# Performance work log

Hardware: AMD Instinct MI355X
Metric: run time of the kernel (lower is better)

## Reference

```python
import jax, jax.numpy as jnp
from jax import lax
import numpy as np

B, T, IN, H = 4096, 200, 79, 10  # batch, seq_len, input_size, hidden_size


def setup_inputs() -> dict:
    key = jax.random.key(0)
    ks = jax.random.split(key, 12)
    f32 = jnp.float32
    return {
        "x": jax.random.normal(ks[0], (B, T, IN), f32),
        # BayesianLSTM reparameterized params: W = mu + softplus(rho) * eps
        "wih_mu": jax.random.normal(ks[1], (IN, 4 * H), f32) * 0.1,
        "wih_rho": jnp.full((IN, 4 * H), -3.0, f32),
        "wih_eps": jax.random.normal(ks[2], (IN, 4 * H), f32),
        "whh_mu": jax.random.normal(ks[3], (H, 4 * H), f32) * 0.1,
        "whh_rho": jnp.full((H, 4 * H), -3.0, f32),
        "whh_eps": jax.random.normal(ks[4], (H, 4 * H), f32),
        "b_mu": jax.random.normal(ks[5], (4 * H,), f32) * 0.1,
        "b_rho": jnp.full((4 * H,), -3.0, f32),
        "b_eps": jax.random.normal(ks[6], (4 * H,), f32),
        # deterministic linear head (10 -> 1)
        "lin_w": jax.random.normal(ks[7], (H, 1), f32) * 0.3,
        "lin_b": jax.random.normal(ks[8], (1,), f32) * 0.1,
    }


def reference(x, wih_mu, wih_rho, wih_eps, whh_mu, whh_rho, whh_eps,
              b_mu, b_rho, b_eps, lin_w, lin_b):
    sp = jax.nn.softplus
    Wih = wih_mu + sp(wih_rho) * wih_eps   # [IN, 4H]
    Whh = whh_mu + sp(whh_rho) * whh_eps   # [H, 4H]
    b = b_mu + sp(b_rho) * b_eps           # [4H]

    # Precompute input projection for all timesteps: [T, B, 4H]
    xg = jnp.einsum('bti,ig->tbg', x, Wih) + b

    h0 = jnp.zeros((x.shape[0], Whh.shape[0]), x.dtype)
    c0 = h0

    def step(carry, g_t):
        h, c = carry
        gates = g_t + h @ Whh
        i, f, g, o = jnp.split(gates, 4, axis=-1)
        i = jax.nn.sigmoid(i)
        f = jax.nn.sigmoid(f)
        g = jnp.tanh(g)
        o = jax.nn.sigmoid(o)
        c = f * c + i * g
        h = o * jnp.tanh(c)
        return (h, c), None

    (hT, _), _ = lax.scan(step, (h0, c0), xg)
    # x_[:, -1, :] == final hidden state hT; then linear head
    return hT @ lin_w + lin_b  # [B, 1]
```

## Files before the change

kernel.cpp:

```cpp
#include <hip/hip_runtime.h>
#include <cstdint>
#include <cmath>

#define Bsz 4096
#define Tlen 200
#define INs 79
#define Hs 10
#define Gs 40
#define LOG2E 1.4426950408889634f

typedef __attribute__((ext_vector_type(8))) short bf16x8;
typedef __attribute__((ext_vector_type(4))) float f32x4;

__device__ __forceinline__ unsigned short f2bf(float x) {
    unsigned u = __float_as_uint(x);
    return (unsigned short)((u + 0x7FFF + ((u >> 16) & 1)) >> 16);
}

__global__ void prep_kernel(const float* __restrict__ wih_mu, const float* __restrict__ wih_rho, const float* __restrict__ wih_eps,
                            const float* __restrict__ whh_mu, const float* __restrict__ whh_rho, const float* __restrict__ whh_eps,
                            const float* __restrict__ b_mu,   const float* __restrict__ b_rho,   const float* __restrict__ b_eps,
                            float* __restrict__ w) {
    int idx = blockIdx.x * 256 + threadIdx.x;
    if (idx < 4608) {
        int c = idx / 96, k = idx % 96;
        float val = 0.0f;
        if (c < Gs && k < INs) {
            int s = k * Gs + c;
            float r = wih_rho[s];
            float sp = (r > 20.0f) ? r : log1pf(expf(r));
            val = fmaf(sp, wih_eps[s], wih_mu[s]);
            val *= (c >= 20 && c < 30) ? -2.0f : -1.0f;
        }
        unsigned short h = f2bf(val);
        float back = __uint_as_float((unsigned)h << 16);
        unsigned short l = f2bf(val - back);
        ((unsigned short*)(w + 512))[idx]  = h;
        ((unsigned short*)(w + 2816))[idx] = l;
    } else if (idx < 5008) {
        int m = idx - 4608;
        float r = whh_rho[m];
        float sp = (r > 20.0f) ? r : log1pf(expf(r));
        w[48 + m] = fmaf(sp, whh_eps[m], whh_mu[m]);
    } else if (idx < 5056) {
        int m = idx - 5008;
        float val = 0.0f;
        if (m < Gs) {
            float r = b_rho[m];
            float sp = (r > 20.0f) ? r : log1pf(expf(r));
            val = fmaf(sp, b_eps[m], b_mu[m]);
            val *= (m >= 20 && m < 30) ? -2.0f : -1.0f;
        }
        w[m] = val;
    }
}

__global__ __launch_bounds__(64, 4) void fused_kernel(
    const float* __restrict__ x, const float* __restrict__ w,
    const float* __restrict__ lin_w, const float* __restrict__ lin_b,
    float* __restrict__ out) {
    __shared__ __align__(16) float sm[1280 + 16 * 42];
    float* xbuf = sm;
    float* gbuf = sm + 1280;

    const int b = blockIdx.x;
    const int lane = threadIdx.x;
    const int jj = lane & 15;
    const int kg8 = (lane >> 4) * 8;

    if (lane < 16) sm[1264 + lane] = 0.0f;

    const unsigned short* Bh = (const unsigned short*)(w + 512);
    const unsigned short* Bl = (const unsigned short*)(w + 2816);

    int pj = (lane & 3) * 10 + (lane >> 2); if (pj > 39) pj = 39;
    const int ty = lane & 3;
    const float sAL = ((ty == 2) ? -2.0f : -1.0f) * LOG2E;
    const float sM  = (ty == 2) ? (-4.0f * LOG2E) : 1.0f;
    const float sC  = (ty == 2) ? ( 2.0f * LOG2E) : 0.0f;
    float wcs[Hs];
#pragma unroll
    for (int k = 0; k < Hs; ++k) wcs[k] = w[48 + k * Gs + pj] * sAL;
    float bias3[3];
#pragma unroll
    for (int n = 0; n < 3; ++n) bias3[n] = w[n * 16 + jj];

    float hs[Hs];
#pragma unroll
    for (int k = 0; k < Hs; ++k) hs[k] = 0.0f;
    float C = 0.0f;

    const long xbaseB = (long)b * (Tlen * INs) * 4;
    const long xendB  = (long)Bsz * Tlen * INs * 4 - 16;
    auto* ldsc = (__attribute__((address_space(3))) char*)xbuf;

    auto stage = [&](int t0) {
        long srcB = xbaseB + (long)t0 * INs * 4;
#pragma unroll
        for (int kk = 0; kk < 4; ++kk) {
            long off = srcB + (long)(kk * 64 + lane) * 16;
            if (off > xendB) off = xendB;
            __builtin_amdgcn_global_load_lds(
                (const __attribute__((address_space(1))) void*)((const char*)x + off),
                (__attribute__((address_space(3))) void*)(ldsc + (kk * 64 + lane) * 16), 16, 0, 0);
        }
        if (lane < 60) {
            long off = srcB + (long)(256 + lane) * 16;
            if (off > xendB) off = xendB;
            __builtin_amdgcn_global_load_lds(
                (const __attribute__((address_space(1))) void*)((const char*)x + off),
                (__attribute__((address_space(3))) void*)(ldsc + (256 + lane) * 16), 16, 0, 0);
        }
    };

    stage(0);

    for (int tile = 0; tile < 13; ++tile) {
        const int t0 = tile * 16;
        asm volatile("s_waitcnt vmcnt(0)" ::: "memory");

        float f0[8], f1[8], f2[8];
#pragma unroll
        for (int e = 0; e < 8; ++e) f0[e] = xbuf[jj * INs + kg8 + e];
#pragma unroll
        for (int e = 0; e < 8; ++e) f1[e] = xbuf[jj * INs + 32 + kg8 + e];
#pragma unroll
        for (int e = 0; e < 8; ++e) {
            float raw = xbuf[jj * INs + 64 + kg8 + e];
            f2[e] = (kg8 + e < 15) ? raw : 0.0f;
        }
        asm volatile("s_waitcnt lgkmcnt(0)" ::: "memory");
        if (tile < 12) stage(t0 + 16);

        union { unsigned u[4]; bf16x8 v; } Ah[3], Al[3];
        const float* fp[3] = {f0, f1, f2};
#pragma unroll
        for (int ks = 0; ks < 3; ++ks) {
#pragma unroll
            for (int p = 0; p < 4; ++p) {
                float a = fp[ks][2 * p], bb = fp[ks][2 * p + 1];
                unsigned ua = __float_as_uint(a), ub = __float_as_uint(bb);
                Ah[ks].u[p] = __builtin_amdgcn_perm(ub, ua, 0x07060302);
                float ra = a  - __uint_as_float(ua & 0xFFFF0000u);
                float rb = bb - __uint_as_float(ub & 0xFFFF0000u);
                unsigned pk;
                asm("v_cvt_pk_bf16_f32 %0, %1, %2" : "=v"(pk) : "v"(ra), "v"(rb));
                Al[ks].u[p] = pk;
            }
        }

        f32x4 acc[3];
#pragma unroll
        for (int n = 0; n < 3; ++n)
            acc[n] = (f32x4){bias3[n], bias3[n], bias3[n], bias3[n]};
        __builtin_amdgcn_s_setprio(1);
#pragma unroll
        for (int ks = 0; ks < 3; ++ks) {
            const int k0 = ks * 32;
#pragma unroll
            for (int n = 0; n < 3; ++n) {
                int boff = (n * 16 + jj) * 96 + k0 + kg8;
                bf16x8 bh = *(const bf16x8*)(Bh + boff);
                bf16x8 bl = *(const bf16x8*)(Bl + boff);
                acc[n] = __builtin_amdgcn_mfma_f32_16x16x32_bf16(Ah[ks].v, bh, acc[n], 0, 0, 0);
                acc[n] = __builtin_amdgcn_mfma_f32_16x16x32_bf16(Ah[ks].v, bl, acc[n], 0, 0, 0);
                acc[n] = __builtin_amdgcn_mfma_f32_16x16x32_bf16(Al[ks].v, bh, acc[n], 0, 0, 0);
            }
        }
        __builtin_amdgcn_s_setprio(0);

#pragma unroll
        for (int n = 0; n < 3; ++n) {
            if (n == 2 && jj >= 8) continue;
#pragma unroll
            for (int r = 0; r < 4; ++r)
                gbuf[((lane >> 4) * 4 + r) * 42 + n * 16 + jj] = acc[n][r];
        }
        float gv[16];
#pragma unroll
        for (int tt = 0; tt < 16; ++tt) gv[tt] = gbuf[tt * 42 + pj] * LOG2E;

#pragma unroll
        for (int tt = 0; tt < 16; ++tt) {
            if (t0 + tt < Tlen) {
                float a0 = gv[tt];
                float a1 = hs[1] * wcs[1];
                a0 = fmaf(hs[0], wcs[0], a0); a1 = fmaf(hs[3], wcs[3], a1);
                a0 = fmaf(hs[2], wcs[2], a0); a1 = fmaf(hs[5], wcs[5], a1);
                a0 = fmaf(hs[4], wcs[4], a0); a1 = fmaf(hs[7], wcs[7], a1);
                a0 = fmaf(hs[6], wcs[6], a0); a1 = fmaf(hs[9], wcs[9], a1);
                a0 = fmaf(hs[8], wcs[8], a0);
                float acs = a0 + a1;
                float e  = exp2f(acs);
                float sg = __builtin_amdgcn_rcpf(1.0f + e);
                float act = fmaf(sg, sM, sC);
                int ai = __float_as_int(act);
                float a1d = __int_as_float(__builtin_amdgcn_mov_dpp(ai, 0xB1, 0xF, 0xF, true));
                float a2d = __int_as_float(__builtin_amdgcn_mov_dpp(ai, 0x4E, 0xF, 0xF, true));
                float a3d = __int_as_float(__builtin_amdgcn_mov_dpp(ai, 0x1B, 0xF, 0xF, true));
                C = fmaf(a1d, C, act * a2d);
                float e2 = exp2f(C);
                float th = fmaf(2.0f, __builtin_amdgcn_rcpf(1.0f + e2), -1.0f);
                float hn = a3d * th;
#pragma unroll
                for (int k = 0; k < Hs; ++k)
                    hs[k] = __int_as_float(__builtin_amdgcn_readlane(__float_as_int(hn), 4 * k));
            }
        }
    }

    if (lane == 0) {
        float o = lin_b[0];
#pragma unroll
        for (int k = 0; k < Hs; ++k) o = fmaf(hs[k], lin_w[k], o);
        out[b] = o;
    }
}

extern "C" void kernel_launch(void* const* d_in, const int* in_sizes, int n_in,
                              void* d_out, int out_size, void* d_ws, size_t ws_size,
                              hipStream_t stream) {
    const float* x = (const float*)d_in[0];
    float* w   = (float*)d_ws;
    float* out = (float*)d_out;

    prep_kernel<<<20, 256, 0, stream>>>(
        (const float*)d_in[1], (const float*)d_in[2], (const float*)d_in[3],
        (const float*)d_in[4], (const float*)d_in[5], (const float*)d_in[6],
        (const float*)d_in[7], (const float*)d_in[8], (const float*)d_in[9], w);

    fused_kernel<<<Bsz, 64, 0, stream>>>(
        x, w, (const float*)d_in[10], (const float*)d_in[11], out);
}
```

Measured before the change: 110.5 us.

## Pack eight batch rows per wavefront and replace readlane broadcast with DPP/swizzle

Each 64-lane block now handles 8 batch rows instead of 1. Every 8-lane group runs one row's recurrence, with each lane computing 5 gate columns and exchanging hidden halves through DPP and ds_swizzle instead of 10 scalar readlanes. Input tiles for all 8 rows are staged through a double-buffered LDS pipeline and projected with MFMA before each 16-step recurrence window. This cuts grid size and serial scalar broadcast cost, and uses more lanes per step. In exchange it adds more per-lane register state and a larger LDS footprint, which could reduce occupancy.

```diff
diff --git a/kernel.cpp b/kernel.cpp
--- a/kernel.cpp
+++ b/kernel.cpp
@@ -55,47 +55,48 @@
     }
 }
 
-__global__ __launch_bounds__(64, 4) void fused_kernel(
+__global__ __launch_bounds__(64) void fused_kernel(
     const float* __restrict__ x, const float* __restrict__ w,
     const float* __restrict__ lin_w, const float* __restrict__ lin_b,
     float* __restrict__ out) {
-    __shared__ __align__(16) float sm[1280 + 16 * 42];
-    float* xbuf = sm;
-    float* gbuf = sm + 1280;
-
-    const int b = blockIdx.x;
+    __shared__ __align__(16) float xb[2][1280];
+    __shared__ __align__(16) float gbuf[8 * 676];
+
     const int lane = threadIdx.x;
+    const int b0 = blockIdx.x * 8;
+
     const int jj = lane & 15;
     const int kg8 = (lane >> 4) * 8;
-
-    if (lane < 16) sm[1264 + lane] = 0.0f;
-
     const unsigned short* Bh = (const unsigned short*)(w + 512);
     const unsigned short* Bl = (const unsigned short*)(w + 2816);
-
-    int pj = (lane & 3) * 10 + (lane >> 2); if (pj > 39) pj = 39;
-    const int ty = lane & 3;
+    float bias3[3];
+#pragma unroll
+    for (int n = 0; n < 3; ++n) bias3[n] = w[n * 16 + jj];
+
+    const int rr = lane >> 3;
+    const int ii = lane & 7;
+    const int ty = ii & 3;
+    const int hf = ii >> 2;
+    const int colb = ty * 10 + hf * 5;
     const float sAL = ((ty == 2) ? -2.0f : -1.0f) * LOG2E;
     const float sM  = (ty == 2) ? (-4.0f * LOG2E) : 1.0f;
     const float sC  = (ty == 2) ? ( 2.0f * LOG2E) : 0.0f;
-    float wcs[Hs];
-#pragma unroll
-    for (int k = 0; k < Hs; ++k) wcs[k] = w[48 + k * Gs + pj] * sAL;
-    float bias3[3];
-#pragma unroll
-    for (int n = 0; n < 3; ++n) bias3[n] = w[n * 16 + jj];
-
-    float hs[Hs];
-#pragma unroll
-    for (int k = 0; k < Hs; ++k) hs[k] = 0.0f;
-    float C = 0.0f;
-
-    const long xbaseB = (long)b * (Tlen * INs) * 4;
-    const long xendB  = (long)Bsz * Tlen * INs * 4 - 16;
-    auto* ldsc = (__attribute__((address_space(3))) char*)xbuf;
-
-    auto stage = [&](int t0) {
-        long srcB = xbaseB + (long)t0 * INs * 4;
+    float wo[5][5], wx[5][5];
+#pragma unroll
+    for (int qp = 0; qp < 5; ++qp)
+#pragma unroll
+        for (int q = 0; q < 5; ++q) {
+            wo[qp][q] = w[48 + (hf * 5 + q) * Gs + colb + qp] * sAL;
+            wx[qp][q] = w[48 + ((1 - hf) * 5 + q) * Gs + colb + qp] * sAL;
+        }
+    float ho[5], hx[5], C[5];
+#pragma unroll
+    for (int q = 0; q < 5; ++q) { ho[q] = 0.0f; hx[q] = 0.0f; C[q] = 0.0f; }
+
+    const long xendB = (long)Bsz * Tlen * INs * 4 - 16;
+    auto stage = [&](int r8, int t0, int buf) {
+        long srcB = ((long)(b0 + r8) * Tlen + t0) * (long)INs * 4;
+        auto* ldsc = (__attribute__((address_space(3))) char*)&xb[buf][0];
 #pragma unroll
         for (int kk = 0; kk < 4; ++kk) {
             long off = srcB + (long)(kk * 64 + lane) * 16;
@@ -104,21 +105,17 @@
                 (const __attribute__((address_space(1))) void*)((const char*)x + off),
                 (__attribute__((address_space(3))) void*)(ldsc + (kk * 64 + lane) * 16), 16, 0, 0);
         }
-        if (lane < 60) {
+        {
             long off = srcB + (long)(256 + lane) * 16;
             if (off > xendB) off = xendB;
-            __builtin_amdgcn_global_load_lds(
-                (const __attribute__((address_space(1))) void*)((const char*)x + off),
-                (__attribute__((address_space(3))) void*)(ldsc + (256 + lane) * 16), 16, 0, 0);
+            if (lane < 60)
+                __builtin_amdgcn_global_load_lds(
+                    (const __attribute__((address_space(1))) void*)((const char*)x + off),
+                    (__attribute__((address_space(3))) void*)(ldsc + (256 + lane) * 16), 16, 0, 0);
         }
     };
 
-    stage(0);
-
-    for (int tile = 0; tile < 13; ++tile) {
-        const int t0 = tile * 16;
-        asm volatile("s_waitcnt vmcnt(0)" ::: "memory");
-
+    auto produce = [&](const float* xbuf, float* gb) {
         float f0[8], f1[8], f2[8];
 #pragma unroll
         for (int e = 0; e < 8; ++e) f0[e] = xbuf[jj * INs + kg8 + e];
@@ -130,8 +127,6 @@
             f2[e] = (kg8 + e < 15) ? raw : 0.0f;
         }
         asm volatile("s_waitcnt lgkmcnt(0)" ::: "memory");
-        if (tile < 12) stage(t0 + 16);
-
         union { unsigned u[4]; bf16x8 v; } Ah[3], Al[3];
         const float* fp[3] = {f0, f1, f2};
 #pragma unroll
@@ -148,12 +143,10 @@
                 Al[ks].u[p] = pk;
             }
         }
-
         f32x4 acc[3];
 #pragma unroll
         for (int n = 0; n < 3; ++n)
             acc[n] = (f32x4){bias3[n], bias3[n], bias3[n], bias3[n]};
-        __builtin_amdgcn_s_setprio(1);
 #pragma unroll
         for (int ks = 0; ks < 3; ++ks) {
             const int k0 = ks * 32;
@@ -167,53 +160,78 @@
                 acc[n] = __builtin_amdgcn_mfma_f32_16x16x32_bf16(Al[ks].v, bh, acc[n], 0, 0, 0);
             }
         }
-        __builtin_amdgcn_s_setprio(0);
-
 #pragma unroll
         for (int n = 0; n < 3; ++n) {
             if (n == 2 && jj >= 8) continue;
 #pragma unroll
             for (int r = 0; r < 4; ++r)
-                gbuf[((lane >> 4) * 4 + r) * 42 + n * 16 + jj] = acc[n][r];
-        }
-        float gv[16];
-#pragma unroll
-        for (int tt = 0; tt < 16; ++tt) gv[tt] = gbuf[tt * 42 + pj] * LOG2E;
-
-#pragma unroll
-        for (int tt = 0; tt < 16; ++tt) {
-            if (t0 + tt < Tlen) {
-                float a0 = gv[tt];
-                float a1 = hs[1] * wcs[1];
-                a0 = fmaf(hs[0], wcs[0], a0); a1 = fmaf(hs[3], wcs[3], a1);
-                a0 = fmaf(hs[2], wcs[2], a0); a1 = fmaf(hs[5], wcs[5], a1);
-                a0 = fmaf(hs[4], wcs[4], a0); a1 = fmaf(hs[7], wcs[7], a1);
-                a0 = fmaf(hs[6], wcs[6], a0); a1 = fmaf(hs[9], wcs[9], a1);
-                a0 = fmaf(hs[8], wcs[8], a0);
-                float acs = a0 + a1;
-                float e  = exp2f(acs);
+                gb[((lane >> 4) * 4 + r) * 42 + n * 16 + jj] = acc[n][r];
+        }
+    };
+
+    const int gvbase = rr * 676 + colb;
+
+    stage(0, 0, 0);
+    for (int wdw = 0; wdw < 13; ++wdw) {
+        for (int r8 = 0; r8 < 8; ++r8) {
+            const bool has_next = !(wdw == 12 && r8 == 7);
+            if (has_next) {
+                int nw = (r8 == 7) ? wdw + 1 : wdw;
+                stage((r8 + 1) & 7, nw * 16, (r8 + 1) & 1);
+                asm volatile("s_waitcnt vmcnt(5)" ::: "memory");
+            } else {
+                asm volatile("s_waitcnt vmcnt(0)" ::: "memory");
+            }
+            produce(&xb[r8 & 1][0], gbuf + r8 * 676);
+        }
+        const int nsteps = (wdw == 12) ? 8 : 16;
+        for (int tt = 0; tt < nsteps; ++tt) {
+            float gv[5];
+#pragma unroll
+            for (int q = 0; q < 5; ++q) gv[q] = gbuf[gvbase + tt * 42 + q] * LOG2E;
+            float pre[5];
+#pragma unroll
+            for (int qp = 0; qp < 5; ++qp) {
+                float a0 = gv[qp];
+                float a1 = ho[0] * wo[qp][0];
+                a0 = fmaf(hx[0], wx[qp][0], a0);
+                a1 = fmaf(hx[1], wx[qp][1], a1);
+                a0 = fmaf(ho[1], wo[qp][1], a0);
+                a1 = fmaf(hx[2], wx[qp][2], a1);
+                a0 = fmaf(ho[2], wo[qp][2], a0);
+                a1 = fmaf(hx[3], wx[qp][3], a1);
+                a0 = fmaf(ho[3], wo[qp][3], a0);
+                a1 = fmaf(hx[4], wx[qp][4], a1);
+                a0 = fmaf(ho[4], wo[qp][4], a0);
+                pre[qp] = a0 + a1;
+            }
+#pragma unroll
+            for (int qp = 0; qp < 5; ++qp) {
+                float e  = exp2f(pre[qp]);
                 float sg = __builtin_amdgcn_rcpf(1.0f + e);
                 float act = fmaf(sg, sM, sC);
                 int ai = __float_as_int(act);
                 float a1d = __int_as_float(__builtin_amdgcn_mov_dpp(ai, 0xB1, 0xF, 0xF, true));
                 float a2d = __int_as_float(__builtin_amdgcn_mov_dpp(ai, 0x4E, 0xF, 0xF, true));
                 float a3d = __int_as_float(__builtin_amdgcn_mov_dpp(ai, 0x1B, 0xF, 0xF, true));
-                C = fmaf(a1d, C, act * a2d);
-                float e2 = exp2f(C);
+                C[qp] = fmaf(a1d, C[qp], act * a2d);
+                float e2 = exp2f(C[qp]);
                 float th = fmaf(2.0f, __builtin_amdgcn_rcpf(1.0f + e2), -1.0f);
                 float hn = a3d * th;
-#pragma unroll
-                for (int k = 0; k < Hs; ++k)
-                    hs[k] = __int_as_float(__builtin_amdgcn_readlane(__float_as_int(hn), 4 * k));
+                int hb = __builtin_amdgcn_mov_dpp(__float_as_int(hn), 0x00, 0xF, 0xF, true);
+                ho[qp] = __int_as_float(hb);
+                hx[qp] = __int_as_float(__builtin_amdgcn_ds_swizzle(hb, 0x101F));
             }
         }
     }
 
-    if (lane == 0) {
+    if (ii == 0) {
         float o = lin_b[0];
 #pragma unroll
-        for (int k = 0; k < Hs; ++k) o = fmaf(hs[k], lin_w[k], o);
-        out[b] = o;
+        for (int q = 0; q < 5; ++q) o = fmaf(ho[q], lin_w[q], o);
+#pragma unroll
+        for (int q = 0; q < 5; ++q) o = fmaf(hx[q], lin_w[5 + q], o);
+        out[b0 + rr] = o;
     }
 }
 
@@ -229,6 +247,6 @@
         (const float*)d_in[4], (const float*)d_in[5], (const float*)d_in[6],
         (const float*)d_in[7], (const float*)d_in[8], (const float*)d_in[9], w);
 
-    fused_kernel<<<Bsz, 64, 0, stream>>>(
+    fused_kernel<<<Bsz / 8, 64, 0, stream>>>(
         x, w, (const float*)d_in[10], (const float*)d_in[11], out);
 }
```

After: 258.0 us. 2.33x slower.
